# Optimization experiments

Measured on AMD Instinct MI355X. Metric: run time of the kernel, lower is better.

Reference implementation:

```python
import jax, jax.numpy as jnp
import numpy as np

D_MODEL = 1024
NUM_HEADS = 16
D_K = D_MODEL // NUM_HEADS
THETA = 10000.0
BATCH, SEQ = 2, 2048


def _rope(xh, pos):
    # xh: (..., h, s, d_k), pos: (s,) int
    half = D_K // 2
    inv_freq = THETA ** (-jnp.arange(half, dtype=jnp.float32) * 2.0 / D_K)  # (half,)
    ang = pos.astype(jnp.float32)[:, None] * inv_freq[None, :]              # (s, half)
    cos, sin = jnp.cos(ang), jnp.sin(ang)
    x1 = xh[..., 0::2]  # (..., h, s, half)
    x2 = xh[..., 1::2]
    r1 = x1 * cos - x2 * sin
    r2 = x1 * sin + x2 * cos
    out = jnp.stack([r1, r2], axis=-1)            # (..., h, s, half, 2)
    return out.reshape(xh.shape)


def setup_inputs() -> dict:
    key = jax.random.key(0)
    k1, k2, k3 = jax.random.split(key, 3)
    scale_qkv = (6.0 / (3 * D_MODEL + D_MODEL)) ** 0.5  # xavier uniform bound
    scale_o = (6.0 / (2 * D_MODEL)) ** 0.5
    return {
        "x": jax.random.normal(k1, (BATCH, SEQ, D_MODEL), dtype=jnp.float32),
        "token_positions": jnp.arange(SEQ, dtype=jnp.int64 if jax.config.jax_enable_x64 else jnp.int32),
        "qkv_proj": jax.random.uniform(k2, (3 * D_MODEL, D_MODEL), jnp.float32, -scale_qkv, scale_qkv),
        "o_proj": jax.random.uniform(k3, (D_MODEL, D_MODEL), jnp.float32, -scale_o, scale_o),
    }


def reference(x, token_positions, qkv_proj, o_proj):
    # fused QKV projection: x @ qkv_proj^T
    qkv = jnp.einsum('bsd,ed->bse', x, qkv_proj)          # (b, s, 3*d_model)
    q, k, v = jnp.split(qkv, 3, axis=-1)

    def to_heads(t):
        b, s, _ = t.shape
        return t.reshape(b, s, NUM_HEADS, D_K).transpose(0, 2, 1, 3)  # (b, h, s, d_k)

    qh, kh, vh = to_heads(q), to_heads(k), to_heads(v)
    qh = _rope(qh, token_positions)
    kh = _rope(kh, token_positions)

    scores = jnp.einsum('bhqd,bhkd->bhqk', qh, kh) / (D_K ** 0.5)
    s = x.shape[-2]
    causal = jnp.tril(jnp.ones((s, s), dtype=bool))
    scores = jnp.where(causal, scores, -jnp.inf)
    attn = jax.nn.softmax(scores, axis=-1)
    out = jnp.einsum('bhqk,bhkd->bhqd', attn, vh)          # (b, h, s, d_k)
    out = out.transpose(0, 2, 1, 3).reshape(x.shape[0], s, D_MODEL)
    return jnp.einsum('bsd,od->bso', out, o_proj)
```

## Files before the change

kernel.cpp:

```cpp
#include <hip/hip_runtime.h>
#include <hip/hip_bf16.h>
#include <math.h>

typedef __bf16 bf16_t;
typedef __attribute__((ext_vector_type(2))) __bf16 bf16x2;
typedef __attribute__((ext_vector_type(4))) __bf16 bf16x4;
typedef __attribute__((ext_vector_type(8))) __bf16 bf16x8;
typedef __attribute__((ext_vector_type(4))) float f32x4;
typedef __attribute__((ext_vector_type(2))) float f32x2;

#define BATCH  2
#define SEQ    2048
#define DMODEL 1024
#define NHEADS 16
#define DK     64

typedef const __attribute__((address_space(1))) void* gas_t;
typedef __attribute__((address_space(3))) void* las_t;

#define X_N (BATCH * SEQ * DMODEL)
#define W_N (3 * DMODEL * DMODEL)
#define O_N (DMODEL * DMODEL)
#define TBL_N (SEQ * 32)

__global__ __launch_bounds__(256) void convert_kernel(
    const float* __restrict__ x, const float* __restrict__ w, const float* __restrict__ o,
    const int* __restrict__ pos,
    bf16_t* __restrict__ xb, bf16_t* __restrict__ wb, bf16_t* __restrict__ ob,
    f32x2* __restrict__ tbl)
{
    if (blockIdx.x >= 4096) {
        const int e  = (blockIdx.x - 4096) * 256 + threadIdx.x;
        const int s  = e >> 5;
        const int dp = e & 31;
        const float ang = (float)pos[s] * exp2f(-(float)dp * 0.4152410118609203f);
        tbl[e] = (f32x2){ __cosf(ang), __sinf(ang) };
        return;
    }
    const int gid = blockIdx.x * 256 + threadIdx.x;
    const float* src; bf16_t* dst; int base = gid * 8;
    if (base < X_N)                { src = x; dst = xb; }
    else if (base < X_N + W_N)     { src = w; dst = wb; base -= X_N; }
    else                           { src = o; dst = ob; base -= X_N + W_N; }
    const f32x4 lo = *(const f32x4*)(src + base);
    const f32x4 hi = *(const f32x4*)(src + base + 4);
    bf16x8 r;
    r[0] = (bf16_t)lo[0]; r[1] = (bf16_t)lo[1]; r[2] = (bf16_t)lo[2]; r[3] = (bf16_t)lo[3];
    r[4] = (bf16_t)hi[0]; r[5] = (bf16_t)hi[1]; r[6] = (bf16_t)hi[2]; r[7] = (bf16_t)hi[3];
    *(bf16x8*)(dst + base) = r;
}

__device__ __forceinline__ void gemm128_body(
    const bf16_t* __restrict__ A, const bf16_t* __restrict__ B,
    int rowBase, int colBase, bf16_t* ldsA, bf16_t* ldsB, f32x4 acc[4][4])
{
    const int tid  = threadIdx.x;
    const int lane = tid & 63;
    const int l15  = lane & 15, quad = lane >> 4;
    const int l7   = l15 & 7;
    const int qr   = ((tid >> 6) >> 1) * 64;
    const int qc   = ((tid >> 6) & 1) * 64;

    const int sr   = tid >> 3;
    const int scol = ((tid & 7) ^ (sr & 7)) * 8;
    const bf16_t* ga = A + (size_t)(rowBase + sr) * DMODEL + scol;
    const bf16_t* gb = B + (size_t)(colBase + sr) * DMODEL + scol;
    const int dd = tid * 8;

    for (int k0 = 0; k0 < DMODEL; k0 += 64) {
        __syncthreads();
#pragma unroll
        for (int u = 0; u < 4; ++u) {
            __builtin_amdgcn_global_load_lds((gas_t)(ga + k0 + (size_t)u * 32 * DMODEL),
                                             (las_t)(ldsA + dd + u * 2048), 16, 0, 0);
            __builtin_amdgcn_global_load_lds((gas_t)(gb + k0 + (size_t)u * 32 * DMODEL),
                                             (las_t)(ldsB + dd + u * 2048), 16, 0, 0);
        }
        __syncthreads();

#pragma unroll
        for (int kk = 0; kk < 2; ++kk) {
            const int sw = ((kk * 4 + quad) ^ l7) * 8;
            bf16x8 af[4], bfr[4];
#pragma unroll
            for (int i = 0; i < 4; ++i)
                af[i] = *(const bf16x8*)&ldsA[(qr + i * 16 + l15) * 64 + sw];
#pragma unroll
            for (int j = 0; j < 4; ++j)
                bfr[j] = *(const bf16x8*)&ldsB[(qc + j * 16 + l15) * 64 + sw];
#pragma unroll
            for (int i = 0; i < 4; ++i)
#pragma unroll
                for (int j = 0; j < 4; ++j)
                    acc[i][j] = __builtin_amdgcn_mfma_f32_16x16x32_bf16(af[i], bfr[j], acc[i][j], 0, 0, 0);
        }
    }
}

__global__ __launch_bounds__(256) void qkv_gemm_kernel(
    const bf16_t* __restrict__ x, const bf16_t* __restrict__ w,
    const f32x2* __restrict__ tbl,
    bf16_t* __restrict__ qo, bf16_t* __restrict__ ko, bf16_t* __restrict__ vt)
{
    __shared__ bf16_t ldsA[128 * 64];
    __shared__ bf16_t ldsB[128 * 64];
    const int rowBase = blockIdx.y * 128;
    const int colBase = blockIdx.x * 128;
    f32x4 acc[4][4] = {};
    gemm128_body(x, w, rowBase, colBase, ldsA, ldsB, acc);

    const int lane = threadIdx.x & 63;
    const int l15 = lane & 15, quad = lane >> 4;
    const int qr = ((threadIdx.x >> 6) >> 1) * 64;
    const int qc = ((threadIdx.x >> 6) & 1) * 64;
#pragma unroll
    for (int j = 0; j < 4; ++j) {
        const int col  = colBase + qc + j * 16 + l15;
        const int part = col >> 10;
        const int h    = (col & 1023) >> 6;
        const int d    = col & 63;
        bf16_t* op = (part == 0) ? qo : (part == 1) ? ko : vt;
        if (part < 2) {
            const float psign = (d & 1) ? 1.f : -1.f;
            const f32x2* trow = tbl + (d >> 1);
#pragma unroll
            for (int i = 0; i < 4; ++i) {
#pragma unroll
                for (int r = 0; r < 4; ++r) {
                    const int m = rowBase + qr + i * 16 + quad * 4 + r;
                    const int b = m >> 11;
                    const int s = m & (SEQ - 1);
                    const f32x2 cs = trow[s * 32];
                    const float v = acc[i][j][r];
                    const float p = __shfl_xor(v, 1);
                    const float res = fmaf(p, psign * cs[1], v * cs[0]);
                    op[((size_t)(b * NHEADS + h) * SEQ + s) * DK + d] = (bf16_t)res;
                }
            }
        } else {
#pragma unroll
            for (int i = 0; i < 4; ++i) {
#pragma unroll
                for (int r = 0; r < 4; ++r) {
                    const int m = rowBase + qr + i * 16 + quad * 4 + r;
                    const int b = m >> 11;
                    const int s = m & (SEQ - 1);
                    const int sp = (s & ~63) | ((s & 15) << 2) | ((s >> 4) & 3);
                    op[(size_t)(b * NHEADS + h) * SEQ * DK + (size_t)d * SEQ + sp]
                        = (bf16_t)acc[i][j][r];
                }
            }
        }
    }
}

__global__ __launch_bounds__(256) void out_gemm_kernel(
    const bf16_t* __restrict__ a, const bf16_t* __restrict__ w, float* __restrict__ out)
{
    __shared__ bf16_t ldsA[128 * 64];
    __shared__ bf16_t ldsB[64 * 64];
    const int tid  = threadIdx.x;
    const int lane = tid & 63;
    const int l15  = lane & 15, quad = lane >> 4;
    const int l7   = l15 & 7;
    const int wv   = tid >> 6;
    const int rowBase = blockIdx.y * 128;
    const int colBase = blockIdx.x * 64;

    const int sr   = tid >> 3;
    const int scol = ((tid & 7) ^ (sr & 7)) * 8;
    const bf16_t* ga = a + (size_t)(rowBase + sr) * DMODEL + scol;
    const bf16_t* gb = w + (size_t)(colBase + sr) * DMODEL + scol;
    const int dd = tid * 8;

    f32x4 acc[2][4] = {};
    for (int k0 = 0; k0 < DMODEL; k0 += 64) {
        __syncthreads();
#pragma unroll
        for (int u = 0; u < 4; ++u)
            __builtin_amdgcn_global_load_lds((gas_t)(ga + k0 + (size_t)u * 32 * DMODEL),
                                             (las_t)(ldsA + dd + u * 2048), 16, 0, 0);
#pragma unroll
        for (int u = 0; u < 2; ++u)
            __builtin_amdgcn_global_load_lds((gas_t)(gb + k0 + (size_t)u * 32 * DMODEL),
                                             (las_t)(ldsB + dd + u * 2048), 16, 0, 0);
        __syncthreads();

#pragma unroll
        for (int kk = 0; kk < 2; ++kk) {
            const int sw = ((kk * 4 + quad) ^ l7) * 8;
            bf16x8 af[2], bfr[4];
#pragma unroll
            for (int i = 0; i < 2; ++i)
                af[i] = *(const bf16x8*)&ldsA[(wv * 32 + i * 16 + l15) * 64 + sw];
#pragma unroll
            for (int j = 0; j < 4; ++j)
                bfr[j] = *(const bf16x8*)&ldsB[(j * 16 + l15) * 64 + sw];
#pragma unroll
            for (int i = 0; i < 2; ++i)
#pragma unroll
                for (int j = 0; j < 4; ++j)
                    acc[i][j] = __builtin_amdgcn_mfma_f32_16x16x32_bf16(af[i], bfr[j], acc[i][j], 0, 0, 0);
        }
    }
#pragma unroll
    for (int i = 0; i < 2; ++i) {
#pragma unroll
        for (int r = 0; r < 4; ++r) {
            const int m = rowBase + wv * 32 + i * 16 + quad * 4 + r;
#pragma unroll
            for (int j = 0; j < 4; ++j)
                out[(size_t)m * DMODEL + colBase + j * 16 + l15] = acc[i][j][r];
        }
    }
}

__global__ __launch_bounds__(512) void attn_kernel(
    const bf16_t* __restrict__ Q, const bf16_t* __restrict__ K,
    const bf16_t* __restrict__ VT, bf16_t* __restrict__ AO)
{
    __shared__ bf16_t Kb[2][64 * 64];
    __shared__ bf16_t Vb[2][64 * 64];
    __shared__ bf16_t Pb[8][16 * 72];

    const int bh = blockIdx.x & 31;
    const int j  = blockIdx.x >> 5;
    const int qb = (j < 8) ? j : 23 - j;
    const int nt = 2 * qb + 2;

    const int tid  = threadIdx.x;
    const int wave = tid >> 6, lane = tid & 63;
    const int l15  = lane & 15, quad = lane >> 4;
    const int q0   = qb * 128 + wave * 16;
    const size_t hb = (size_t)bh * SEQ * DK;

    const int sr = tid >> 3;
    const int sc = ((tid & 7) ^ (sr & 7)) * 8;
    const int dd = tid * 8;

    bf16x8 aq0, aq1;
    {
        const bf16_t* qrow = Q + hb + (size_t)(q0 + l15) * DK + quad * 8;
        aq0 = *(const bf16x8*)qrow;
        aq1 = *(const bf16x8*)(qrow + 32);
#pragma unroll
        for (int i = 0; i < 8; ++i) {
            aq0[i] = (bf16_t)((float)aq0[i] * 0.125f);
            aq1[i] = (bf16_t)((float)aq1[i] * 0.125f);
        }
    }

    f32x4 oacc[4] = {};
    float lsum[4] = {};

    __builtin_amdgcn_global_load_lds((gas_t)(K  + hb + (size_t)sr * DK + sc),
                                     (las_t)(&Kb[0][dd]), 16, 0, 0);
    __builtin_amdgcn_global_load_lds((gas_t)(VT + hb + (size_t)sr * SEQ + sc),
                                     (las_t)(&Vb[0][dd]), 16, 0, 0);
    __syncthreads();

    const int swA = (quad ^ (l15 & 7)) * 8;
    const int swB = ((4 + quad) ^ (l15 & 7)) * 8;

    int buf = 0;
    for (int kb = 0; kb < nt; ++kb) {
        if (kb + 1 < nt) {
            const bf16_t* kg = K  + hb + (size_t)(kb + 1) * 64 * DK;
            const bf16_t* vg = VT + hb + (kb + 1) * 64;
            __builtin_amdgcn_global_load_lds((gas_t)(kg + (size_t)sr * DK + sc),
                                             (las_t)(&Kb[buf ^ 1][dd]), 16, 0, 0);
            __builtin_amdgcn_global_load_lds((gas_t)(vg + (size_t)sr * SEQ + sc),
                                             (las_t)(&Vb[buf ^ 1][dd]), 16, 0, 0);
        }

        const bool act = (kb * 64 <= q0 + 15);
        const bool nm  = (kb * 64 + 63 > q0);

        if (act) {
            bf16x8 kf0[4], kf1[4];
#pragma unroll
            for (int c = 0; c < 4; ++c) {
                kf0[c] = *(const bf16x8*)&Kb[buf][(c * 16 + l15) * 64 + swA];
                kf1[c] = *(const bf16x8*)&Kb[buf][(c * 16 + l15) * 64 + swB];
            }
            f32x4 sc4[4];
#pragma unroll
            for (int c = 0; c < 4; ++c) {
                f32x4 z = {};
                z = __builtin_amdgcn_mfma_f32_16x16x32_bf16(aq0, kf0[c], z, 0, 0, 0);
                z = __builtin_amdgcn_mfma_f32_16x16x32_bf16(aq1, kf1[c], z, 0, 0, 0);
                sc4[c] = z;
            }
#pragma unroll
            for (int r = 0; r < 4; ++r) {
                bf16x4 pr;
#pragma unroll
                for (int c = 0; c < 4; ++c) {
                    float s = sc4[c][r];
                    if (nm) {
                        const int key = kb * 64 + c * 16 + l15;
                        const int qa  = q0 + quad * 4 + r;
                        s = (key <= qa) ? s : -INFINITY;
                    }
                    const float p = __expf(s - 8.0f);
                    lsum[r] += p;
                    pr[c] = (bf16_t)p;
                }
                *(bf16x4*)&Pb[wave][(quad * 4 + r) * 72 + l15 * 4] = pr;
            }
            asm volatile("s_waitcnt lgkmcnt(0)" ::: "memory");

            const bf16x8 ap0 = *(const bf16x8*)&Pb[wave][l15 * 72 + quad * 8];
            const bf16x8 ap1 = *(const bf16x8*)&Pb[wave][l15 * 72 + 32 + quad * 8];
#pragma unroll
            for (int t = 0; t < 4; ++t) {
                const bf16x8 bv0 = *(const bf16x8*)&Vb[buf][(t * 16 + l15) * 64 + swA];
                const bf16x8 bv1 = *(const bf16x8*)&Vb[buf][(t * 16 + l15) * 64 + swB];
                oacc[t] = __builtin_amdgcn_mfma_f32_16x16x32_bf16(ap0, bv0, oacc[t], 0, 0, 0);
                oacc[t] = __builtin_amdgcn_mfma_f32_16x16x32_bf16(ap1, bv1, oacc[t], 0, 0, 0);
            }
        }

        __syncthreads();
        buf ^= 1;
    }

    const int b = bh >> 4, h = bh & 15;
    float inv[4];
#pragma unroll
    for (int r = 0; r < 4; ++r) {
        float s = lsum[r];
        s += __shfl_xor(s, 1);
        s += __shfl_xor(s, 2);
        s += __shfl_xor(s, 4);
        s += __shfl_xor(s, 8);
        inv[r] = 1.0f / s;
    }
#pragma unroll
    for (int t = 0; t < 4; ++t)
#pragma unroll
        for (int r = 0; r < 4; ++r) {
            const int qa = q0 + quad * 4 + r;
            AO[(size_t)(b * SEQ + qa) * DMODEL + h * 64 + t * 16 + l15] =
                (bf16_t)(oacc[t][r] * inv[r]);
        }
}

extern "C" void kernel_launch(void* const* d_in, const int* in_sizes, int n_in,
                              void* d_out, int out_size, void* d_ws, size_t ws_size,
                              hipStream_t stream) {
    (void)in_sizes; (void)n_in; (void)out_size; (void)ws_size;
    const float* x    = (const float*)d_in[0];
    const int*   pos  = (const int*)d_in[1];
    const float* qkvw = (const float*)d_in[2];
    const float* ow   = (const float*)d_in[3];
    float* out = (float*)d_out;

    const size_t HEAD_ELEMS = (size_t)BATCH * NHEADS * SEQ * DK;
    bf16_t* Qw  = (bf16_t*)d_ws;
    bf16_t* Kw  = Qw + HEAD_ELEMS;
    bf16_t* Vt  = Kw + HEAD_ELEMS;
    bf16_t* AO  = Vt + HEAD_ELEMS;
    bf16_t* xb  = AO;
    bf16_t* wb  = AO + X_N;
    bf16_t* ob  = wb + W_N;
    f32x2*  tbl = (f32x2*)(ob + O_N);

    convert_kernel<<<dim3(4096 + 256), 256, 0, stream>>>(x, qkvw, ow, pos, xb, wb, ob, tbl);
    qkv_gemm_kernel<<<dim3(24, 32), 256, 0, stream>>>(xb, wb, tbl, Qw, Kw, Vt);
    attn_kernel<<<dim3(512), 512, 0, stream>>>(Qw, Kw, Vt, AO);
    out_gemm_kernel<<<dim3(16, 32), 256, 0, stream>>>(AO, ob, out);
}
```

Baseline: 184.5 us.

## Double-buffer LDS tiles in QKV and output GEMMs to overlap loads with MFMA

Both projection GEMMs now use two LDS buffers. The next K-slice is issued with global_load_lds before the current slice's MFMAs run, and each iteration has one barrier instead of two. This is meant to hide global-memory latency behind compute. LDS use per block doubles, to 64KB for the QKV GEMM, which may reduce occupancy. Correctness relies on the barrier at the end of each iteration also waiting for the outstanding async LDS loads.

```diff
diff --git a/kernel.cpp b/kernel.cpp
--- a/kernel.cpp
+++ b/kernel.cpp
@@ -21,7 +21,6 @@
 #define X_N (BATCH * SEQ * DMODEL)
 #define W_N (3 * DMODEL * DMODEL)
 #define O_N (DMODEL * DMODEL)
-#define TBL_N (SEQ * 32)
 
 __global__ __launch_bounds__(256) void convert_kernel(
     const float* __restrict__ x, const float* __restrict__ w, const float* __restrict__ o,
@@ -67,33 +66,47 @@
     const bf16_t* gb = B + (size_t)(colBase + sr) * DMODEL + scol;
     const int dd = tid * 8;
 
+#pragma unroll
+    for (int u = 0; u < 4; ++u) {
+        __builtin_amdgcn_global_load_lds((gas_t)(ga + (size_t)u * 32 * DMODEL),
+                                         (las_t)(ldsA + dd + u * 2048), 16, 0, 0);
+        __builtin_amdgcn_global_load_lds((gas_t)(gb + (size_t)u * 32 * DMODEL),
+                                         (las_t)(ldsB + dd + u * 2048), 16, 0, 0);
+    }
+    __syncthreads();
+
+    int buf = 0;
     for (int k0 = 0; k0 < DMODEL; k0 += 64) {
-        __syncthreads();
-#pragma unroll
-        for (int u = 0; u < 4; ++u) {
-            __builtin_amdgcn_global_load_lds((gas_t)(ga + k0 + (size_t)u * 32 * DMODEL),
-                                             (las_t)(ldsA + dd + u * 2048), 16, 0, 0);
-            __builtin_amdgcn_global_load_lds((gas_t)(gb + k0 + (size_t)u * 32 * DMODEL),
-                                             (las_t)(ldsB + dd + u * 2048), 16, 0, 0);
-        }
-        __syncthreads();
-
+        if (k0 + 64 < DMODEL) {
+            const int off = (buf ^ 1) * 8192;
+#pragma unroll
+            for (int u = 0; u < 4; ++u) {
+                __builtin_amdgcn_global_load_lds((gas_t)(ga + k0 + 64 + (size_t)u * 32 * DMODEL),
+                                                 (las_t)(ldsA + off + dd + u * 2048), 16, 0, 0);
+                __builtin_amdgcn_global_load_lds((gas_t)(gb + k0 + 64 + (size_t)u * 32 * DMODEL),
+                                                 (las_t)(ldsB + off + dd + u * 2048), 16, 0, 0);
+            }
+        }
+        const bf16_t* La = ldsA + buf * 8192;
+        const bf16_t* Lb = ldsB + buf * 8192;
 #pragma unroll
         for (int kk = 0; kk < 2; ++kk) {
             const int sw = ((kk * 4 + quad) ^ l7) * 8;
             bf16x8 af[4], bfr[4];
 #pragma unroll
             for (int i = 0; i < 4; ++i)
-                af[i] = *(const bf16x8*)&ldsA[(qr + i * 16 + l15) * 64 + sw];
+                af[i] = *(const bf16x8*)&La[(qr + i * 16 + l15) * 64 + sw];
 #pragma unroll
             for (int j = 0; j < 4; ++j)
-                bfr[j] = *(const bf16x8*)&ldsB[(qc + j * 16 + l15) * 64 + sw];
+                bfr[j] = *(const bf16x8*)&Lb[(qc + j * 16 + l15) * 64 + sw];
 #pragma unroll
             for (int i = 0; i < 4; ++i)
 #pragma unroll
                 for (int j = 0; j < 4; ++j)
                     acc[i][j] = __builtin_amdgcn_mfma_f32_16x16x32_bf16(af[i], bfr[j], acc[i][j], 0, 0, 0);
         }
+        __syncthreads();
+        buf ^= 1;
     }
 }
 
@@ -102,8 +115,8 @@
     const f32x2* __restrict__ tbl,
     bf16_t* __restrict__ qo, bf16_t* __restrict__ ko, bf16_t* __restrict__ vt)
 {
-    __shared__ bf16_t ldsA[128 * 64];
-    __shared__ bf16_t ldsB[128 * 64];
+    __shared__ bf16_t ldsA[2 * 128 * 64];
+    __shared__ bf16_t ldsB[2 * 128 * 64];
     const int rowBase = blockIdx.y * 128;
     const int colBase = blockIdx.x * 128;
     f32x4 acc[4][4] = {};
@@ -157,8 +170,8 @@
 __global__ __launch_bounds__(256) void out_gemm_kernel(
     const bf16_t* __restrict__ a, const bf16_t* __restrict__ w, float* __restrict__ out)
 {
-    __shared__ bf16_t ldsA[128 * 64];
-    __shared__ bf16_t ldsB[64 * 64];
+    __shared__ bf16_t ldsA[2 * 128 * 64];
+    __shared__ bf16_t ldsB[2 * 64 * 64];
     const int tid  = threadIdx.x;
     const int lane = tid & 63;
     const int l15  = lane & 15, quad = lane >> 4;
@@ -173,35 +186,50 @@
     const bf16_t* gb = w + (size_t)(colBase + sr) * DMODEL + scol;
     const int dd = tid * 8;
 
+#pragma unroll
+    for (int u = 0; u < 4; ++u)
+        __builtin_amdgcn_global_load_lds((gas_t)(ga + (size_t)u * 32 * DMODEL),
+                                         (las_t)(ldsA + dd + u * 2048), 16, 0, 0);
+#pragma unroll
+    for (int u = 0; u < 2; ++u)
+        __builtin_amdgcn_global_load_lds((gas_t)(gb + (size_t)u * 32 * DMODEL),
+                                         (las_t)(ldsB + dd + u * 2048), 16, 0, 0);
+    __syncthreads();
+
     f32x4 acc[2][4] = {};
+    int buf = 0;
     for (int k0 = 0; k0 < DMODEL; k0 += 64) {
-        __syncthreads();
-#pragma unroll
-        for (int u = 0; u < 4; ++u)
-            __builtin_amdgcn_global_load_lds((gas_t)(ga + k0 + (size_t)u * 32 * DMODEL),
-                                             (las_t)(ldsA + dd + u * 2048), 16, 0, 0);
-#pragma unroll
-        for (int u = 0; u < 2; ++u)
-            __builtin_amdgcn_global_load_lds((gas_t)(gb + k0 + (size_t)u * 32 * DMODEL),
-                                             (las_t)(ldsB + dd + u * 2048), 16, 0, 0);
-        __syncthreads();
-
+        if (k0 + 64 < DMODEL) {
+            const int offA = (buf ^ 1) * 8192, offB = (buf ^ 1) * 4096;
+#pragma unroll
+            for (int u = 0; u < 4; ++u)
+                __builtin_amdgcn_global_load_lds((gas_t)(ga + k0 + 64 + (size_t)u * 32 * DMODEL),
+                                                 (las_t)(ldsA + offA + dd + u * 2048), 16, 0, 0);
+#pragma unroll
+            for (int u = 0; u < 2; ++u)
+                __builtin_amdgcn_global_load_lds((gas_t)(gb + k0 + 64 + (size_t)u * 32 * DMODEL),
+                                                 (las_t)(ldsB + offB + dd + u * 2048), 16, 0, 0);
+        }
+        const bf16_t* La = ldsA + buf * 8192;
+        const bf16_t* Lb = ldsB + buf * 4096;
 #pragma unroll
         for (int kk = 0; kk < 2; ++kk) {
             const int sw = ((kk * 4 + quad) ^ l7) * 8;
             bf16x8 af[2], bfr[4];
 #pragma unroll
             for (int i = 0; i < 2; ++i)
-                af[i] = *(const bf16x8*)&ldsA[(wv * 32 + i * 16 + l15) * 64 + sw];
+                af[i] = *(const bf16x8*)&La[(wv * 32 + i * 16 + l15) * 64 + sw];
 #pragma unroll
             for (int j = 0; j < 4; ++j)
-                bfr[j] = *(const bf16x8*)&ldsB[(j * 16 + l15) * 64 + sw];
+                bfr[j] = *(const bf16x8*)&Lb[(j * 16 + l15) * 64 + sw];
 #pragma unroll
             for (int i = 0; i < 2; ++i)
 #pragma unroll
                 for (int j = 0; j < 4; ++j)
                     acc[i][j] = __builtin_amdgcn_mfma_f32_16x16x32_bf16(af[i], bfr[j], acc[i][j], 0, 0, 0);
         }
+        __syncthreads();
+        buf ^= 1;
     }
 #pragma unroll
     for (int i = 0; i < 2; ++i) {
```

Measured after the change: 184.2 us. No clear change (-0.1%).
